# Kernel optimization log

Hardware: AMD Instinct MI355X
Metric: run time of the kernel (lower is better)

## Reference

```python
import jax, jax.numpy as jnp
import numpy as np

N_NODES = 100000
N_EDGES = 1600000
NUM_RELS = 16
NUM_BASES = 8
IN_FEATS = 128
N_HIDDEN = 128
N_CLASSES = 40


def _make_layer_params(key, d_in, d_out):
    k0, k1, k2 = jax.random.split(key, 3)
    s_in = 1.0 / np.sqrt(d_in)
    bases = jax.random.normal(k0, (NUM_BASES, d_in, d_out), jnp.float32) * s_in
    comp = jax.random.normal(k1, (NUM_RELS, NUM_BASES), jnp.float32) * (1.0 / np.sqrt(NUM_BASES))
    root = jax.random.normal(k2, (d_in, d_out), jnp.float32) * s_in
    bias = jnp.zeros((d_out,), jnp.float32)
    return bases, comp, root, bias


def setup_inputs() -> dict:
    key = jax.random.key(0)
    ks = jax.random.split(key, 8)
    x = jax.random.normal(ks[0], (N_NODES, IN_FEATS), jnp.float32)
    edge_src = jax.random.randint(ks[1], (N_EDGES,), 0, N_NODES, dtype=jnp.int32)
    edge_dst = jax.random.randint(ks[2], (N_EDGES,), 0, N_NODES, dtype=jnp.int32)
    edge_type = jax.random.randint(ks[3], (N_EDGES,), 0, NUM_RELS, dtype=jnp.int32)
    bases0, comp0, root0, bias0 = _make_layer_params(ks[4], IN_FEATS, N_HIDDEN)
    bases1, comp1, root1, bias1 = _make_layer_params(ks[5], N_HIDDEN, N_HIDDEN)
    bases2, comp2, root2, bias2 = _make_layer_params(ks[6], N_HIDDEN, N_CLASSES)
    return dict(x=x, edge_src=edge_src, edge_dst=edge_dst, edge_type=edge_type,
                bases0=bases0, comp0=comp0, root0=root0, bias0=bias0,
                bases1=bases1, comp1=comp1, root1=root1, bias1=bias1,
                bases2=bases2, comp2=comp2, root2=root2, bias2=bias2)


def _rgcn_layer(x, edge_src, edge_dst, edge_type, bases, comp, root, bias):
    # basis decomposition: W_r = sum_b comp[r,b] * bases[b]   -> [R, d_in, d_out]
    W = jnp.einsum('rb,bio->rio', comp, bases)
    # transform all node features under every relation (R small, dense GEMMs)
    xw = jnp.einsum('ni,rio->rno', x, W)                    # [R, N, d_out]
    # per-edge message: gather by (relation, source) -- irregular access
    msg = xw[edge_type, edge_src]                           # [E, d_out]
    # mean aggregation per (destination, relation), as in PyG RGCNConv (aggr='mean')
    seg = edge_dst * NUM_RELS + edge_type                   # [E]
    deg = jax.ops.segment_sum(jnp.ones((msg.shape[0],), x.dtype), seg,
                              num_segments=N_NODES * NUM_RELS)
    norm = 1.0 / jnp.maximum(deg[seg], 1.0)                 # [E]
    agg = jax.ops.segment_sum(msg * norm[:, None], edge_dst, num_segments=N_NODES)
    return agg + x @ root + bias


def reference(x, edge_src, edge_dst, edge_type,
              bases0, comp0, root0, bias0,
              bases1, comp1, root1, bias1,
              bases2, comp2, root2, bias2):
    # dropout is identity at inference; activation='relu' on all but last layer
    h = _rgcn_layer(x, edge_src, edge_dst, edge_type, bases0, comp0, root0, bias0)
    h = jax.nn.relu(h)
    h = _rgcn_layer(h, edge_src, edge_dst, edge_type, bases1, comp1, root1, bias1)
    h = jax.nn.relu(h)
    h = _rgcn_layer(h, edge_src, edge_dst, edge_type, bases2, comp2, root2, bias2)
    return h
```

## Files before the change

### kernel.cpp

```cpp
#include <hip/hip_runtime.h>
#include <hip/hip_bf16.h>

#define NNODES 100000
#define NEDGES 1600000
#define NRELS 16
#define NBASES 8
#define DFEAT 128
#define NCLS 40
#define MAXDEG 64
#define KTOT 1152

typedef __attribute__((ext_vector_type(8))) short bf16x8v;
typedef __attribute__((ext_vector_type(4))) float f32x4v;
typedef __attribute__((ext_vector_type(2))) float f32x2v;

struct __align__(8) bf16x4s { __hip_bfloat162 lo, hi; };

__global__ __launch_bounds__(256)
void k_cvq(const float* __restrict__ x, __hip_bfloat16* __restrict__ xb,
           short* __restrict__ q8, float* __restrict__ qs, int nrows)
{
    int wave = threadIdx.x >> 6, lane = threadIdx.x & 63;
    int v = blockIdx.x * 4 + wave;
    if (v >= nrows) return;
    float2 xv = ((const float2*)x)[(size_t)v * 64 + lane];
    __hip_bfloat162 bv;
    bv.x = __float2bfloat16(xv.x);
    bv.y = __float2bfloat16(xv.y);
    ((__hip_bfloat162*)xb)[(size_t)v * 64 + lane] = bv;
    float m = fmaxf(fabsf(xv.x), fabsf(xv.y));
#pragma unroll
    for (int o = 32; o; o >>= 1) m = fmaxf(m, __shfl_xor(m, o));
    float inv = (m > 0.f) ? 127.f / m : 0.f;
    int qx = (int)rintf(xv.x * inv), qy = (int)rintf(xv.y * inv);
    q8[(size_t)v * 64 + lane] = (short)((qx & 0xff) | (qy << 8));
    if (lane == 0) qs[v] = m * (1.f / 127.f);
}

__global__ __launch_bounds__(256)
void k_build(const int* __restrict__ esrc, const int* __restrict__ edst,
             const int* __restrict__ etyp,
             unsigned* __restrict__ degD, unsigned* __restrict__ ell)
{
    int e = blockIdx.x * 256 + threadIdx.x;
    if (e >= NEDGES) return;
    int d = edst[e], t = etyp[e], s = esrc[e];
    unsigned slot = atomicAdd(&degD[d], 1u);
    if (slot < MAXDEG) ell[(size_t)d * MAXDEG + slot] = ((unsigned)s << 4) | (unsigned)t;
}

__global__ __launch_bounds__(256)
void k_quant(const __hip_bfloat16* __restrict__ h,
             short* __restrict__ q8, float* __restrict__ qs, int nrows)
{
    int wave = threadIdx.x >> 6, lane = threadIdx.x & 63;
    int v = blockIdx.x * 4 + wave;
    if (v >= nrows) return;
    __hip_bfloat162 xv = ((const __hip_bfloat162*)h)[(size_t)v * 64 + lane];
    float xl = __bfloat162float(xv.x), xh = __bfloat162float(xv.y);
    float m = fmaxf(fabsf(xl), fabsf(xh));
#pragma unroll
    for (int o = 32; o; o >>= 1) m = fmaxf(m, __shfl_xor(m, o));
    float inv = (m > 0.f) ? 127.f / m : 0.f;
    int qx = (int)rintf(xl * inv), qy = (int)rintf(xh * inv);
    q8[(size_t)v * 64 + lane] = (short)((qx & 0xff) | (qy << 8));
    if (lane == 0) qs[v] = m * (1.f / 127.f);
}

__global__ __launch_bounds__(256)
void k_agg(const short* __restrict__ q8, const float* __restrict__ qs,
           const __hip_bfloat16* __restrict__ hin,
           const unsigned* __restrict__ ell,
           const unsigned* __restrict__ degD,
           const float* __restrict__ comp,
           __hip_bfloat16* __restrict__ A,
           int r0, int rows)
{
    __shared__ float compS[NRELS * NBASES];
    __shared__ __align__(16) float cS[8][MAXDEG][8];
    __shared__ unsigned sS[8][MAXDEG];
    __shared__ unsigned histS[8][NRELS];
    if (threadIdx.x < NRELS * NBASES) compS[threadIdx.x] = comp[threadIdx.x];
    __syncthreads();

    int wave = threadIdx.x >> 6, lane = threadIdx.x & 63;
    int half = lane >> 5, hl = lane & 31;
    int node = wave * 2 + half;
    int rl = blockIdx.x * 8 + node;
    bool alive = (rl < rows);
    int v = alive ? (r0 + rl) : 0;
    int ne = alive ? (int)degD[v] : 0; if (ne > MAXDEG) ne = MAXDEG;

    if (alive) {
        const unsigned* erow = ell + (size_t)v * MAXDEG;
        unsigned p0 = (hl < ne) ? erow[hl] : 0u;
        unsigned p1 = (hl + 32 < ne) ? erow[hl + 32] : 0u;
        if (hl < NRELS) histS[node][hl] = 0u;
        if (hl < ne)      atomicAdd(&histS[node][p0 & 15u], 1u);
        if (hl + 32 < ne) atomicAdd(&histS[node][p1 & 15u], 1u);
#pragma unroll
        for (int r = 0; r < 2; r++) {
            unsigned p = r ? p1 : p0;
            int slot = hl + 32 * r;
            bool val = (slot < ne);
            unsigned t = p & 15u;
            int s = val ? (int)(p >> 4) : 0;
            unsigned cnt = val ? histS[node][t] : 1u;
            if (cnt < 1u) cnt = 1u;
            float w = val ? (qs[s] / (float)cnt) : 0.f;
            f32x4v c0, c1;
#pragma unroll
            for (int b = 0; b < 4; b++) c0[b] = compS[t * NBASES + b] * w;
#pragma unroll
            for (int b = 0; b < 4; b++) c1[b] = compS[t * NBASES + 4 + b] * w;
            *(f32x4v*)&cS[node][slot][0] = c0;
            *(f32x4v*)&cS[node][slot][4] = c1;
            sS[node][slot] = (unsigned)s;
        }
    }

    f32x2v accA[NBASES], accB[NBASES];
#pragma unroll
    for (int b = 0; b < NBASES; b++) { accA[b] = (f32x2v){0.f,0.f}; accB[b] = (f32x2v){0.f,0.f}; }

    if (alive) {
        for (int e0 = 0; e0 < ne; e0 += 16) {
            unsigned qd[16];
#pragma unroll
            for (int j = 0; j < 16; j++) {
                unsigned s = sS[node][e0 + j];
                qd[j] = ((const unsigned*)(q8 + (size_t)s * 64))[hl];
            }
#pragma unroll
            for (int j = 0; j < 16; j++) {
                f32x4v ca = *(const f32x4v*)&cS[node][e0 + j][0];
                f32x4v cb = *(const f32x4v*)&cS[node][e0 + j][4];
                unsigned d = qd[j];
                f32x2v f01, f23;
                f01.x = (float)(char)(d & 0xff);
                f01.y = (float)(char)((d >> 8) & 0xff);
                f23.x = (float)(char)((d >> 16) & 0xff);
                f23.y = (float)(char)(d >> 24);
                accA[0] += ca[0] * f01;  accB[0] += ca[0] * f23;
                accA[1] += ca[1] * f01;  accB[1] += ca[1] * f23;
                accA[2] += ca[2] * f01;  accB[2] += ca[2] * f23;
                accA[3] += ca[3] * f01;  accB[3] += ca[3] * f23;
                accA[4] += cb[0] * f01;  accB[4] += cb[0] * f23;
                accA[5] += cb[1] * f01;  accB[5] += cb[1] * f23;
                accA[6] += cb[2] * f01;  accB[6] += cb[2] * f23;
                accA[7] += cb[3] * f01;  accB[7] += cb[3] * f23;
            }
        }
        __hip_bfloat16* Arow = A + (size_t)rl * KTOT;
#pragma unroll
        for (int b = 0; b < NBASES; b++) {
            bf16x4s o;
            o.lo.x = __float2bfloat16(accA[b].x);
            o.lo.y = __float2bfloat16(accA[b].y);
            o.hi.x = __float2bfloat16(accB[b].x);
            o.hi.y = __float2bfloat16(accB[b].y);
            *(bf16x4s*)&Arow[b * 128 + 4 * hl] = o;
        }
        *(bf16x4s*)&Arow[1024 + 4 * hl] =
            *(const bf16x4s*)&hin[(size_t)v * 128 + 4 * hl];
    }
}

__global__ __launch_bounds__(256)
void k_w(const float* __restrict__ bases, const float* __restrict__ root,
         __hip_bfloat16* __restrict__ WT, int dout, int npad)
{
    int idx = blockIdx.x * 256 + threadIdx.x;
    int total = npad * KTOT;
    if (idx >= total) return;
    int o = idx / KTOT, k = idx - o * KTOT;
    float v = 0.f;
    if (o < dout) v = (k < 1024) ? bases[k * dout + o] : root[(k - 1024) * dout + o];
    WT[idx] = __float2bfloat16(v);
}

template<int NT, bool RELU, bool FINAL>
__global__ __launch_bounds__(256)
void k_gemm(const __hip_bfloat16* __restrict__ A,
            const __hip_bfloat16* __restrict__ WT,
            const float* __restrict__ bias,
            void* __restrict__ outp,
            int r0, int rows, int dout)
{
    constexpr int WM = (NT == 128) ? 2 : 4;
    constexpr int WN = 4 / WM;
    constexpr int MT = 128 / (16 * WM);
    constexpr int NTW = NT / (16 * WN);
    __shared__ __align__(16) __hip_bfloat16 As[128 * 32];
    __shared__ __align__(16) __hip_bfloat16 Bs[NT * 32];
    int tid = threadIdx.x;
    int wave = tid >> 6, lane = tid & 63;
    int wm = wave % WM, wn = wave / WM;
    int bm = blockIdx.x * 128;
    int lm = lane & 15, lq = lane >> 4;
    f32x4v zero = {0.f, 0.f, 0.f, 0.f};
    f32x4v acc[MT][NTW];
#pragma unroll
    for (int a = 0; a < MT; a++)
#pragma unroll
        for (int b = 0; b < NTW; b++) acc[a][b] = zero;

    for (int k0 = 0; k0 < KTOT; k0 += 32) {
#pragma unroll
        for (int j = 0; j < 2; j++) {
            int slot = tid + 256 * j;
            int row = slot >> 2, kc = (slot & 3) << 3;
            __builtin_amdgcn_global_load_lds(
                (const __attribute__((address_space(1))) void*)
                    &A[(size_t)(bm + row) * KTOT + k0 + kc],
                (__attribute__((address_space(3))) void*)&As[slot * 8],
                16, 0, 0);
        }
#pragma unroll
        for (int j = 0; j < NT / 64; j++) {
            int slot = tid + 256 * j;
            int row = slot >> 2, kc = (slot & 3) << 3;
            __builtin_amdgcn_global_load_lds(
                (const __attribute__((address_space(1))) void*)
                    &WT[(size_t)row * KTOT + k0 + kc],
                (__attribute__((address_space(3))) void*)&Bs[slot * 8],
                16, 0, 0);
        }
        __syncthreads();
        bf16x8v af[MT], bfr[NTW];
#pragma unroll
        for (int mt = 0; mt < MT; mt++)
            af[mt] = *(const bf16x8v*)&As[(wm * (16 * MT) + mt * 16 + lm) * 32 + lq * 8];
#pragma unroll
        for (int nt = 0; nt < NTW; nt++)
            bfr[nt] = *(const bf16x8v*)&Bs[(wn * (16 * NTW) + nt * 16 + lm) * 32 + lq * 8];
#pragma unroll
        for (int mt = 0; mt < MT; mt++)
#pragma unroll
            for (int nt = 0; nt < NTW; nt++)
                acc[mt][nt] = __builtin_amdgcn_mfma_f32_16x16x32_bf16(
                    af[mt], bfr[nt], acc[mt][nt], 0, 0, 0);
        __syncthreads();
    }
#pragma unroll
    for (int mt = 0; mt < MT; mt++) {
        int rbase = bm + wm * (16 * MT) + mt * 16 + lq * 4;
#pragma unroll
        for (int nt = 0; nt < NTW; nt++) {
            int col = wn * (16 * NTW) + nt * 16 + lm;
#pragma unroll
            for (int i = 0; i < 4; i++) {
                int rl = rbase + i;
                if (rl < rows && col < dout) {
                    float v = acc[mt][nt][i] + bias[col];
                    if (RELU) v = fmaxf(v, 0.f);
                    if (FINAL)
                        ((float*)outp)[(size_t)(r0 + rl) * NCLS + col] = v;
                    else
                        ((__hip_bfloat16*)outp)[(size_t)(r0 + rl) * DFEAT + col] =
                            __float2bfloat16(v);
                }
            }
        }
    }
}

extern "C" void kernel_launch(void* const* d_in, const int* in_sizes, int n_in,
                              void* d_out, int out_size, void* d_ws, size_t ws_size,
                              hipStream_t stream)
{
    const float* x  = (const float*)d_in[0];
    const int* esrc = (const int*)d_in[1];
    const int* edst = (const int*)d_in[2];
    const int* etyp = (const int*)d_in[3];
    const float* basesA[3] = {(const float*)d_in[4], (const float*)d_in[8], (const float*)d_in[12]};
    const float* compA[3]  = {(const float*)d_in[5], (const float*)d_in[9], (const float*)d_in[13]};
    const float* rootA[3]  = {(const float*)d_in[6], (const float*)d_in[10], (const float*)d_in[14]};
    const float* biasA[3]  = {(const float*)d_in[7], (const float*)d_in[11], (const float*)d_in[15]};

    size_t off = 0;
    char* base = (char*)d_ws;
    auto carve = [&](size_t bytes) -> void* {
        void* r = base + off;
        off += (bytes + 255) & ~(size_t)255;
        return r;
    };
    __hip_bfloat16* xb = (__hip_bfloat16*)carve((size_t)NNODES * DFEAT * 2);
    __hip_bfloat16* h1 = (__hip_bfloat16*)carve((size_t)NNODES * DFEAT * 2);
    __hip_bfloat16* WT = (__hip_bfloat16*)carve((size_t)128 * KTOT * 2);
    unsigned* ell  = (unsigned*)carve((size_t)NNODES * MAXDEG * 4);
    unsigned* degD = (unsigned*)carve((size_t)NNODES * 4);
    short* q8  = (short*)carve((size_t)NNODES * 64 * 2);
    float* qsc = (float*)carve((size_t)NNODES * 4);
    __hip_bfloat16* h2 = xb;

    if (ws_size <= off) return;
    size_t arows = (ws_size - off) / ((size_t)KTOT * 2);
    if (arows > 100096) arows = 100096;
    int chunk = (int)(arows & ~(size_t)127);
    if (chunk < 128) return;
    __hip_bfloat16* A = (__hip_bfloat16*)(base + off);

    hipMemsetAsync(degD, 0, (size_t)NNODES * 4, stream);
    k_cvq<<<(NNODES + 3) / 4, 256, 0, stream>>>(x, xb, q8, qsc, NNODES);
    k_build<<<(NEDGES + 255) / 256, 256, 0, stream>>>(esrc, edst, etyp, degD, ell);

    const __hip_bfloat16* hin = xb;
    __hip_bfloat16* houts[2] = {h1, h2};
    for (int l = 0; l < 3; l++) {
        int dout = (l == 2) ? NCLS : DFEAT;
        int npad = (l == 2) ? 64 : 128;
        if (l > 0)
            k_quant<<<(NNODES + 3) / 4, 256, 0, stream>>>(hin, q8, qsc, NNODES);
        k_w<<<(npad * KTOT + 255) / 256, 256, 0, stream>>>(basesA[l], rootA[l], WT, dout, npad);
        for (int r0 = 0; r0 < NNODES; r0 += chunk) {
            int rows = NNODES - r0; if (rows > chunk) rows = chunk;
            k_agg<<<(rows + 7) / 8, 256, 0, stream>>>(q8, qsc, hin, ell, degD, compA[l], A, r0, rows);
            int gm = (rows + 127) / 128;
            if (l < 2)
                k_gemm<128, true, false><<<gm, 256, 0, stream>>>(A, WT, biasA[l], houts[l], r0, rows, dout);
            else
                k_gemm<64, false, true><<<gm, 256, 0, stream>>>(A, WT, biasA[l], d_out, r0, rows, dout);
        }
        if (l < 2) hin = houts[l];
    }
}
```

Before: 763.1 us.

## Fuse quantization into GEMM epilogue, read root input directly, merge preprocessing kernels

The GEMM epilogue now computes the per-row max through LDS atomics and writes the int8 quantized activations and their scales, so the separate quantization kernels are gone. The GEMM loads the root-term K slice straight from the previous layer's activations instead of having the aggregation kernel copy it into A, which shrinks A to 1024 columns. The x conversion and ELL build kernels are merged into one launch with interleaved block roles, and A and ELL writes use nontemporal stores. The cost is extra epilogue work, a block-level barrier and double-buffered quantization arrays.

```diff
diff --git a/kernel.cpp b/kernel.cpp
--- a/kernel.cpp
+++ b/kernel.cpp
@@ -9,67 +9,65 @@
 #define NCLS 40
 #define MAXDEG 64
 #define KTOT 1152
+#define KA   1024
 
 typedef __attribute__((ext_vector_type(8))) short bf16x8v;
 typedef __attribute__((ext_vector_type(4))) float f32x4v;
 typedef __attribute__((ext_vector_type(2))) float f32x2v;
+typedef __attribute__((ext_vector_type(4))) unsigned short u16x4;
 
 struct __align__(8) bf16x4s { __hip_bfloat162 lo, hi; };
 
 __global__ __launch_bounds__(256)
-void k_cvq(const float* __restrict__ x, __hip_bfloat16* __restrict__ xb,
-           short* __restrict__ q8, float* __restrict__ qs, int nrows)
-{
-    int wave = threadIdx.x >> 6, lane = threadIdx.x & 63;
-    int v = blockIdx.x * 4 + wave;
-    if (v >= nrows) return;
-    float2 xv = ((const float2*)x)[(size_t)v * 64 + lane];
-    __hip_bfloat162 bv;
-    bv.x = __float2bfloat16(xv.x);
-    bv.y = __float2bfloat16(xv.y);
-    ((__hip_bfloat162*)xb)[(size_t)v * 64 + lane] = bv;
-    float m = fmaxf(fabsf(xv.x), fabsf(xv.y));
-#pragma unroll
-    for (int o = 32; o; o >>= 1) m = fmaxf(m, __shfl_xor(m, o));
-    float inv = (m > 0.f) ? 127.f / m : 0.f;
-    int qx = (int)rintf(xv.x * inv), qy = (int)rintf(xv.y * inv);
-    q8[(size_t)v * 64 + lane] = (short)((qx & 0xff) | (qy << 8));
-    if (lane == 0) qs[v] = m * (1.f / 127.f);
-}
-
-__global__ __launch_bounds__(256)
-void k_build(const int* __restrict__ esrc, const int* __restrict__ edst,
-             const int* __restrict__ etyp,
-             unsigned* __restrict__ degD, unsigned* __restrict__ ell)
-{
-    int e = blockIdx.x * 256 + threadIdx.x;
-    if (e >= NEDGES) return;
-    int d = edst[e], t = etyp[e], s = esrc[e];
-    unsigned slot = atomicAdd(&degD[d], 1u);
-    if (slot < MAXDEG) ell[(size_t)d * MAXDEG + slot] = ((unsigned)s << 4) | (unsigned)t;
-}
-
-__global__ __launch_bounds__(256)
-void k_quant(const __hip_bfloat16* __restrict__ h,
-             short* __restrict__ q8, float* __restrict__ qs, int nrows)
-{
-    int wave = threadIdx.x >> 6, lane = threadIdx.x & 63;
-    int v = blockIdx.x * 4 + wave;
-    if (v >= nrows) return;
-    __hip_bfloat162 xv = ((const __hip_bfloat162*)h)[(size_t)v * 64 + lane];
-    float xl = __bfloat162float(xv.x), xh = __bfloat162float(xv.y);
-    float m = fmaxf(fabsf(xl), fabsf(xh));
-#pragma unroll
-    for (int o = 32; o; o >>= 1) m = fmaxf(m, __shfl_xor(m, o));
-    float inv = (m > 0.f) ? 127.f / m : 0.f;
-    int qx = (int)rintf(xl * inv), qy = (int)rintf(xh * inv);
-    q8[(size_t)v * 64 + lane] = (short)((qx & 0xff) | (qy << 8));
-    if (lane == 0) qs[v] = m * (1.f / 127.f);
+void k_pre(const float* __restrict__ x, __hip_bfloat16* __restrict__ xb,
+           short* __restrict__ q8, float* __restrict__ qs,
+           const int* __restrict__ esrc, const int* __restrict__ edst,
+           const int* __restrict__ etyp,
+           unsigned* __restrict__ degD, unsigned* __restrict__ ell)
+{
+    unsigned bid = blockIdx.x;
+    if (bid % 17u == 0u) {
+        int k = (int)(bid / 17u);
+        int e0 = k * 1024 + ((int)threadIdx.x << 2);
+        if (e0 < NEDGES) {
+            int4 s4 = *(const int4*)(esrc + e0);
+            int4 d4 = *(const int4*)(edst + e0);
+            int4 t4 = *(const int4*)(etyp + e0);
+            unsigned sl0 = atomicAdd(&degD[d4.x], 1u);
+            unsigned sl1 = atomicAdd(&degD[d4.y], 1u);
+            unsigned sl2 = atomicAdd(&degD[d4.z], 1u);
+            unsigned sl3 = atomicAdd(&degD[d4.w], 1u);
+            if (sl0 < MAXDEG) __builtin_nontemporal_store(
+                ((unsigned)s4.x << 4) | (unsigned)t4.x, &ell[(size_t)d4.x * MAXDEG + sl0]);
+            if (sl1 < MAXDEG) __builtin_nontemporal_store(
+                ((unsigned)s4.y << 4) | (unsigned)t4.y, &ell[(size_t)d4.y * MAXDEG + sl1]);
+            if (sl2 < MAXDEG) __builtin_nontemporal_store(
+                ((unsigned)s4.z << 4) | (unsigned)t4.z, &ell[(size_t)d4.z * MAXDEG + sl2]);
+            if (sl3 < MAXDEG) __builtin_nontemporal_store(
+                ((unsigned)s4.w << 4) | (unsigned)t4.w, &ell[(size_t)d4.w * MAXDEG + sl3]);
+        }
+    } else {
+        int cb = (int)(bid - (bid + 16u) / 17u);
+        int wave = threadIdx.x >> 6, lane = threadIdx.x & 63;
+        int v = cb * 4 + wave;
+        if (v >= NNODES) return;
+        float2 xv = ((const float2*)x)[(size_t)v * 64 + lane];
+        __hip_bfloat162 bv;
+        bv.x = __float2bfloat16(xv.x);
+        bv.y = __float2bfloat16(xv.y);
+        ((__hip_bfloat162*)xb)[(size_t)v * 64 + lane] = bv;
+        float m = fmaxf(fabsf(xv.x), fabsf(xv.y));
+#pragma unroll
+        for (int o = 32; o; o >>= 1) m = fmaxf(m, __shfl_xor(m, o));
+        float inv = (m > 0.f) ? 127.f / m : 0.f;
+        int qx = (int)rintf(xv.x * inv), qy = (int)rintf(xv.y * inv);
+        q8[(size_t)v * 64 + lane] = (short)((qx & 0xff) | (qy << 8));
+        if (lane == 0) qs[v] = m * (1.f / 127.f);
+    }
 }
 
 __global__ __launch_bounds__(256)
 void k_agg(const short* __restrict__ q8, const float* __restrict__ qs,
-           const __hip_bfloat16* __restrict__ hin,
            const unsigned* __restrict__ ell,
            const unsigned* __restrict__ degD,
            const float* __restrict__ comp,
@@ -151,7 +149,7 @@
                 accA[7] += cb[3] * f01;  accB[7] += cb[3] * f23;
             }
         }
-        __hip_bfloat16* Arow = A + (size_t)rl * KTOT;
+        __hip_bfloat16* Arow = A + (size_t)rl * KA;
 #pragma unroll
         for (int b = 0; b < NBASES; b++) {
             bf16x4s o;
@@ -159,10 +157,8 @@
             o.lo.y = __float2bfloat16(accA[b].y);
             o.hi.x = __float2bfloat16(accB[b].x);
             o.hi.y = __float2bfloat16(accB[b].y);
-            *(bf16x4s*)&Arow[b * 128 + 4 * hl] = o;
-        }
-        *(bf16x4s*)&Arow[1024 + 4 * hl] =
-            *(const bf16x4s*)&hin[(size_t)v * 128 + 4 * hl];
+            __builtin_nontemporal_store(*(const u16x4*)&o, (u16x4*)&Arow[b * 128 + 4 * hl]);
+        }
     }
 }
 
@@ -175,16 +171,18 @@
     if (idx >= total) return;
     int o = idx / KTOT, k = idx - o * KTOT;
     float v = 0.f;
-    if (o < dout) v = (k < 1024) ? bases[k * dout + o] : root[(k - 1024) * dout + o];
+    if (o < dout) v = (k < KA) ? bases[k * dout + o] : root[(k - KA) * dout + o];
     WT[idx] = __float2bfloat16(v);
 }
 
 template<int NT, bool RELU, bool FINAL>
 __global__ __launch_bounds__(256)
 void k_gemm(const __hip_bfloat16* __restrict__ A,
+            const __hip_bfloat16* __restrict__ hroot,
             const __hip_bfloat16* __restrict__ WT,
             const float* __restrict__ bias,
             void* __restrict__ outp,
+            short* __restrict__ q8o, float* __restrict__ qso,
             int r0, int rows, int dout)
 {
     constexpr int WM = (NT == 128) ? 2 : 4;
@@ -193,11 +191,13 @@
     constexpr int NTW = NT / (16 * WN);
     __shared__ __align__(16) __hip_bfloat16 As[128 * 32];
     __shared__ __align__(16) __hip_bfloat16 Bs[NT * 32];
+    __shared__ unsigned rmax[128];
     int tid = threadIdx.x;
     int wave = tid >> 6, lane = tid & 63;
     int wm = wave % WM, wn = wave / WM;
     int bm = blockIdx.x * 128;
     int lm = lane & 15, lq = lane >> 4;
+    if (RELU && tid < 128) rmax[tid] = 0u;
     f32x4v zero = {0.f, 0.f, 0.f, 0.f};
     f32x4v acc[MT][NTW];
 #pragma unroll
@@ -210,9 +210,15 @@
         for (int j = 0; j < 2; j++) {
             int slot = tid + 256 * j;
             int row = slot >> 2, kc = (slot & 3) << 3;
+            const __hip_bfloat16* src;
+            if (k0 < KA) {
+                src = &A[(size_t)(bm + row) * KA + k0 + kc];
+            } else {
+                int gr = r0 + bm + row; if (gr > NNODES - 1) gr = NNODES - 1;
+                src = &hroot[(size_t)gr * DFEAT + (k0 - KA) + kc];
+            }
             __builtin_amdgcn_global_load_lds(
-                (const __attribute__((address_space(1))) void*)
-                    &A[(size_t)(bm + row) * KTOT + k0 + kc],
+                (const __attribute__((address_space(1))) void*)src,
                 (__attribute__((address_space(3))) void*)&As[slot * 8],
                 16, 0, 0);
         }
@@ -242,26 +248,57 @@
                     af[mt], bfr[nt], acc[mt][nt], 0, 0, 0);
         __syncthreads();
     }
+
+#pragma unroll
+    for (int mt = 0; mt < MT; mt++) {
+#pragma unroll
+        for (int i = 0; i < 4; i++) {
+            float mx = 0.f;
+#pragma unroll
+            for (int nt = 0; nt < NTW; nt++) {
+                int col = wn * (16 * NTW) + nt * 16 + lm;
+                float v = acc[mt][nt][i] + bias[col];
+                if (RELU) { v = fmaxf(v, 0.f); mx = fmaxf(mx, v); }
+                acc[mt][nt][i] = v;
+            }
+            if (RELU) {
+                int lrow = wm * (16 * MT) + mt * 16 + lq * 4 + i;
+                atomicMax(&rmax[lrow], __float_as_uint(mx));
+            }
+        }
+    }
+    if (RELU) __syncthreads();
 #pragma unroll
     for (int mt = 0; mt < MT; mt++) {
         int rbase = bm + wm * (16 * MT) + mt * 16 + lq * 4;
 #pragma unroll
-        for (int nt = 0; nt < NTW; nt++) {
-            int col = wn * (16 * NTW) + nt * 16 + lm;
-#pragma unroll
-            for (int i = 0; i < 4; i++) {
-                int rl = rbase + i;
-                if (rl < rows && col < dout) {
-                    float v = acc[mt][nt][i] + bias[col];
-                    if (RELU) v = fmaxf(v, 0.f);
-                    if (FINAL)
+        for (int i = 0; i < 4; i++) {
+            int rl = rbase + i;
+            if (rl >= rows) continue;
+            float inv = 0.f;
+            if (RELU) {
+                float m = __uint_as_float(rmax[wm * (16 * MT) + mt * 16 + lq * 4 + i]);
+                inv = (m > 0.f) ? 127.f / m : 0.f;
+            }
+#pragma unroll
+            for (int nt = 0; nt < NTW; nt++) {
+                int col = wn * (16 * NTW) + nt * 16 + lm;
+                float v = acc[mt][nt][i];
+                if (FINAL) {
+                    if (col < dout)
                         ((float*)outp)[(size_t)(r0 + rl) * NCLS + col] = v;
-                    else
-                        ((__hip_bfloat16*)outp)[(size_t)(r0 + rl) * DFEAT + col] =
-                            __float2bfloat16(v);
+                } else {
+                    ((__hip_bfloat16*)outp)[(size_t)(r0 + rl) * DFEAT + col] =
+                        __float2bfloat16(v);
+                    int qv = (int)rintf(v * inv);
+                    ((char*)q8o)[(size_t)(r0 + rl) * DFEAT + col] = (char)qv;
                 }
             }
         }
+    }
+    if (RELU) {
+        if (tid < 128 && bm + tid < rows)
+            qso[r0 + bm + tid] = __uint_as_float(rmax[tid]) * (1.f / 127.f);
     }
 }
 
@@ -290,38 +327,44 @@
     __hip_bfloat16* WT = (__hip_bfloat16*)carve((size_t)128 * KTOT * 2);
     unsigned* ell  = (unsigned*)carve((size_t)NNODES * MAXDEG * 4);
     unsigned* degD = (unsigned*)carve((size_t)NNODES * 4);
-    short* q8  = (short*)carve((size_t)NNODES * 64 * 2);
-    float* qsc = (float*)carve((size_t)NNODES * 4);
-    __hip_bfloat16* h2 = xb;
+    short* q8A = (short*)carve((size_t)NNODES * 64 * 2);
+    short* q8B = (short*)carve((size_t)NNODES * 64 * 2);
+    float* qsA = (float*)carve((size_t)NNODES * 4);
+    float* qsB = (float*)carve((size_t)NNODES * 4);
 
     if (ws_size <= off) return;
-    size_t arows = (ws_size - off) / ((size_t)KTOT * 2);
+    size_t arows = (ws_size - off) / ((size_t)KA * 2);
     if (arows > 100096) arows = 100096;
     int chunk = (int)(arows & ~(size_t)127);
     if (chunk < 128) return;
     __hip_bfloat16* A = (__hip_bfloat16*)(base + off);
 
     hipMemsetAsync(degD, 0, (size_t)NNODES * 4, stream);
-    k_cvq<<<(NNODES + 3) / 4, 256, 0, stream>>>(x, xb, q8, qsc, NNODES);
-    k_build<<<(NEDGES + 255) / 256, 256, 0, stream>>>(esrc, edst, etyp, degD, ell);
+    k_pre<<<26563, 256, 0, stream>>>(x, xb, q8A, qsA, esrc, edst, etyp, degD, ell);
 
     const __hip_bfloat16* hin = xb;
-    __hip_bfloat16* houts[2] = {h1, h2};
+    __hip_bfloat16* houts[2] = {h1, xb};
+    const short* q8in = q8A;  short* q8out = q8B;
+    const float* qsin = qsA;  float* qsout = qsB;
     for (int l = 0; l < 3; l++) {
         int dout = (l == 2) ? NCLS : DFEAT;
         int npad = (l == 2) ? 64 : 128;
-        if (l > 0)
-            k_quant<<<(NNODES + 3) / 4, 256, 0, stream>>>(hin, q8, qsc, NNODES);
         k_w<<<(npad * KTOT + 255) / 256, 256, 0, stream>>>(basesA[l], rootA[l], WT, dout, npad);
         for (int r0 = 0; r0 < NNODES; r0 += chunk) {
             int rows = NNODES - r0; if (rows > chunk) rows = chunk;
-            k_agg<<<(rows + 7) / 8, 256, 0, stream>>>(q8, qsc, hin, ell, degD, compA[l], A, r0, rows);
+            k_agg<<<(rows + 7) / 8, 256, 0, stream>>>(q8in, qsin, ell, degD, compA[l], A, r0, rows);
             int gm = (rows + 127) / 128;
             if (l < 2)
-                k_gemm<128, true, false><<<gm, 256, 0, stream>>>(A, WT, biasA[l], houts[l], r0, rows, dout);
+                k_gemm<128, true, false><<<gm, 256, 0, stream>>>(
+                    A, hin, WT, biasA[l], houts[l], q8out, qsout, r0, rows, dout);
             else
-                k_gemm<64, false, true><<<gm, 256, 0, stream>>>(A, WT, biasA[l], d_out, r0, rows, dout);
-        }
-        if (l < 2) hin = houts[l];
-    }
-}
+                k_gemm<64, false, true><<<gm, 256, 0, stream>>>(
+                    A, hin, WT, biasA[l], d_out, nullptr, nullptr, r0, rows, dout);
+        }
+        if (l < 2) {
+            hin = houts[l];
+            const short* tq = q8in; q8in = q8out; q8out = (short*)tq;
+            const float* tf = qsin; qsin = qsout; qsout = (float*)tf;
+        }
+    }
+}
```

New measurement: 741.8 us. -2.8%, faster.
